# Kernel tuning notes

Measured on AMD Instinct MI355X. Metric: run time of the kernel, lower is better.

## Reference

```python
import jax, jax.numpy as jnp
import numpy as np


def _chamfer_pair(x, y):
    # x: [N,3], y: [M,3] -> per-point squared NN distances (dist1 [N], dist2 [M])
    # d_ij = |x_i|^2 + |y_j|^2 - 2 x_i . y_j
    d = (jnp.sum(x * x, axis=1)[:, None]
         + jnp.sum(y * y, axis=1)[None, :]
         - 2.0 * (x @ y.T))  # [N, M]
    return jnp.min(d, axis=1), jnp.min(d, axis=0)


def setup_inputs() -> dict:
    key = jax.random.key(0)
    k1, k2 = jax.random.split(key)
    B, N, M = 4, 8192, 8192
    xyz1 = jax.random.normal(k1, (B, N, 3), dtype=jnp.float32)
    xyz2 = jax.random.normal(k2, (B, M, 3), dtype=jnp.float32)
    return {"xyz1": xyz1, "xyz2": xyz2}


def reference(xyz1, xyz2):
    # lax.map over batch keeps peak memory to one [N,M] matrix at a time,
    # mirroring the tiled custom-kernel structure of ChamferFunction.
    dist1, dist2 = jax.lax.map(lambda ab: _chamfer_pair(ab[0], ab[1]), (xyz1, xyz2))
    return jnp.mean(dist1) + jnp.mean(dist2)
```

## Files before the change

### kernel.cpp

```cpp
#include <hip/hip_runtime.h>


#define BATCH 4
#define NPTS 8192
#define TPB 1024
#define GRID 256
#define XBLKS 32
#define YQ 2048
#define CHUNK 512
#define NCHUNK 4
#define JT 16

typedef __attribute__((ext_vector_type(8))) short bf16x8;
typedef __attribute__((ext_vector_type(16))) float f32x16;
union FragU { int4 i4; bf16x8 v; };

__device__ inline unsigned short bf16_rne(float f) {
    unsigned int u = __float_as_uint(f);
    return (unsigned short)((u + 0x7FFFu + ((u >> 16) & 1u)) >> 16);
}
__device__ inline float bf16_f32(unsigned short h) {
    return __uint_as_float(((unsigned int)h) << 16);
}
__device__ inline unsigned int pack2(unsigned int lo, unsigned int hi) {
    return (lo & 0xFFFFu) | (hi << 16);
}

__device__ inline float red16(float cb, const f32x16& d) {
    const float m0 = fminf(fminf(d[0],  d[1]),  d[2]);
    const float m1 = fminf(fminf(d[3],  d[4]),  d[5]);
    const float m2 = fminf(fminf(d[6],  d[7]),  d[8]);
    const float m3 = fminf(fminf(d[9],  d[10]), d[11]);
    const float m4 = fminf(fminf(d[12], d[13]), d[14]);
    const float u0 = fminf(fminf(m0, m1), m2);
    const float u1 = fminf(fminf(m3, m4), d[15]);
    return fminf(fminf(cb, u0), u1);
}

__device__ inline void pack_row(float x0, float x1, float x2,
                                int4& rlo, int4& rhi) {
    const unsigned short h0 = bf16_rne(x0), h1 = bf16_rne(x1), h2 = bf16_rne(x2);
    const unsigned short l0 = bf16_rne(x0 - bf16_f32(h0));
    const unsigned short l1 = bf16_rne(x1 - bf16_f32(h1));
    const unsigned short l2 = bf16_rne(x2 - bf16_f32(h2));
    const float s = x0 * x0 + x1 * x1 + x2 * x2;
    const unsigned short sh = bf16_rne(s);
    const unsigned short sl = bf16_rne(s - bf16_f32(sh));
    const unsigned short one = 0x3F80;
    rlo.x = pack2(h0, h1); rlo.y = pack2(h2, h0);
    rlo.z = pack2(h1, h2); rlo.w = pack2(l0, l1);
    rhi.x = pack2(l2, one); rhi.y = pack2(one, sh);
    rhi.z = pack2(sl, 0u);  rhi.w = 0;
}

__device__ inline void pack_col(float x0, float x1, float x2,
                                int4& clo, int4& chi) {
    const float s = x0 * x0 + x1 * x1 + x2 * x2;
    const unsigned short sh = bf16_rne(s);
    const unsigned short sl = bf16_rne(s - bf16_f32(sh));
    const float g0 = -2.0f * x0, g1 = -2.0f * x1, g2 = -2.0f * x2;
    const unsigned short gh0 = bf16_rne(g0), gh1 = bf16_rne(g1), gh2 = bf16_rne(g2);
    const unsigned short gl0 = bf16_rne(g0 - bf16_f32(gh0));
    const unsigned short gl1 = bf16_rne(g1 - bf16_f32(gh1));
    const unsigned short gl2 = bf16_rne(g2 - bf16_f32(gh2));
    const unsigned short one = 0x3F80;
    clo.x = pack2(gh0, gh1); clo.y = pack2(gh2, gl0);
    clo.z = pack2(gl1, gl2); clo.w = pack2(gh0, gh1);
    chi.x = pack2(gh2, sh);  chi.y = pack2(sl, one);
    chi.z = pack2(one, 0u);  chi.w = 0;
}

__global__ __launch_bounds__(TPB) void chamfer_one(
    const float* __restrict__ xyz1,
    const float* __restrict__ xyz2,
    unsigned long long* __restrict__ partials,
    unsigned int* __restrict__ counter,
    float* __restrict__ out)
{
    const int blk  = blockIdx.x;
    const int xblk = blk & (XBLKS - 1);
    const int b    = (blk >> 5) & (BATCH - 1);
    const int dir  = blk >> 7;

    const float* colsrc = dir ? xyz2 : xyz1;
    const float* rowsrc = dir ? xyz1 : xyz2;

    const int t    = threadIdx.x;
    const int lane = t & 63;
    const int w    = t >> 6;
    const int g    = w >> 2;
    const int wl   = w & 3;
    const int half = lane >> 5, l31 = lane & 31;

    __shared__ int4  sb0[4][CHUNK];
    __shared__ int4  sb1[4][CHUNK];
    __shared__ float part[4][256];
    __shared__ double red[16];
    __shared__ unsigned int lastflag;

    FragU bf0, bf1;
    {
        const int cbase = xblk * 256 + wl * 64 + l31;
        const float* p0 = colsrc + ((size_t)b * NPTS + cbase) * 3;
        const float* p1 = colsrc + ((size_t)b * NPTS + cbase + 32) * 3;
        int4 clo, chi;
        pack_col(p0[0], p0[1], p0[2], clo, chi);
        bf0.i4 = half ? chi : clo;
        pack_col(p1[0], p1[1], p1[2], clo, chi);
        bf1.i4 = half ? chi : clo;
    }

    float cb0 = __builtin_inff();
    float cb1 = __builtin_inff();
    const f32x16 zero = {0.0f, 0.0f, 0.0f, 0.0f, 0.0f, 0.0f, 0.0f, 0.0f,
                         0.0f, 0.0f, 0.0f, 0.0f, 0.0f, 0.0f, 0.0f, 0.0f};

    const int tid256 = t & 255;
    const int sg     = t >> 8;
    const float* rbase = rowsrc + ((size_t)b * NPTS + (size_t)sg * YQ) * 3;

    for (int c = 0; c < NCHUNK; ++c) {
        __syncthreads();
        {
            const int p = tid256 * 2;
            const float* s0 = rbase + ((size_t)c * CHUNK + p) * 3;
            int4 rlo, rhi;
            pack_row(s0[0], s0[1], s0[2], rlo, rhi);
            sb0[sg][p]     = rlo;  sb1[sg][p]     = rhi;
            pack_row(s0[3], s0[4], s0[5], rlo, rhi);
            sb0[sg][p + 1] = rlo;  sb1[sg][p + 1] = rhi;
        }
        __syncthreads();

        const int4* asrc = half ? sb1[g] : sb0[g];
#pragma unroll 4
        for (int jt = 0; jt < JT; ++jt) {
            FragU af; af.i4 = asrc[jt * 32 + l31];
            f32x16 d0 = __builtin_amdgcn_mfma_f32_32x32x16_bf16(af.v, bf0.v, zero, 0, 0, 0);
            f32x16 d1 = __builtin_amdgcn_mfma_f32_32x32x16_bf16(af.v, bf1.v, zero, 0, 0, 0);
            cb0 = red16(cb0, d0);
            cb1 = red16(cb1, d1);
        }
    }

    {
        const float v0 = fminf(cb0, __shfl_xor(cb0, 32, 64));
        const float v1 = fminf(cb1, __shfl_xor(cb1, 32, 64));
        if (half == 0) {
            part[g][wl * 64 + l31]      = v0;
            part[g][wl * 64 + 32 + l31] = v1;
        }
    }
    __syncthreads();

    double s = 0.0;
    if (t < 256) {
        const float m = fminf(fminf(part[0][t], part[1][t]),
                              fminf(part[2][t], part[3][t]));
        s = (double)m;
    }
    for (int off = 32; off > 0; off >>= 1) s += __shfl_down(s, off, 64);
    if ((t & 63) == 0) red[w] = s;
    __syncthreads();
    if (t == 0) {
        double bs = 0.0;
        for (int i = 0; i < 16; ++i) bs += red[i];
        atomicExch(&partials[blk], (unsigned long long)__double_as_longlong(bs));
        __threadfence();
        lastflag = (atomicAdd(counter, 1u) == GRID - 1) ? 1u : 0u;
    }
    __syncthreads();

    if (lastflag) {
        if (w == 0) {
            double fs = 0.0;
#pragma unroll
            for (int i = 0; i < 4; ++i) {
                const unsigned long long pv =
                    atomicAdd(&partials[lane * 4 + i], 0ull);
                fs += __longlong_as_double((long long)pv);
            }
            for (int off = 32; off > 0; off >>= 1) fs += __shfl_down(fs, off, 64);
            if (lane == 0)
                out[0] = (float)(fs / (double)(BATCH * NPTS));
        }
    }
}

extern "C" void kernel_launch(void* const* d_in, const int* in_sizes, int n_in,
                              void* d_out, int out_size, void* d_ws, size_t ws_size,
                              hipStream_t stream) {
    const float* xyz1 = (const float*)d_in[0];
    const float* xyz2 = (const float*)d_in[1];
    float* out = (float*)d_out;

    unsigned long long* partials = (unsigned long long*)d_ws;
    unsigned int* counter = (unsigned int*)(partials + GRID);

    hipMemsetAsync(counter, 0, sizeof(unsigned int), stream);

    chamfer_one<<<GRID, TPB, 0, stream>>>(xyz1, xyz2, partials, counter, out);
}
```

Baseline: 36.59 us.

## Prepack bf16 split operands in a separate kernel and stream rows from global

```diff
diff --git a/kernel.cpp b/kernel.cpp
--- a/kernel.cpp
+++ b/kernel.cpp
@@ -3,13 +3,12 @@
 
 #define BATCH 4
 #define NPTS 8192
-#define TPB 1024
-#define GRID 256
-#define XBLKS 32
-#define YQ 2048
-#define CHUNK 512
-#define NCHUNK 4
-#define JT 16
+#define TPB 512
+#define GRID 512
+#define XBLKS 64
+#define COLS_PER_BLOCK 128
+#define ROWS_PER_GROUP 2048
+#define JT 64
 
 typedef __attribute__((ext_vector_type(8))) short bf16x8;
 typedef __attribute__((ext_vector_type(16))) float f32x16;
@@ -26,6 +25,50 @@
     return (lo & 0xFFFFu) | (hi << 16);
 }
 
+__global__ __launch_bounds__(256) void prepack_kernel(
+    const float* __restrict__ xyz1, const float* __restrict__ xyz2,
+    int4* __restrict__ rowpack, int4* __restrict__ colpack,
+    unsigned int* __restrict__ counter)
+{
+    const int id  = blockIdx.x * 256 + threadIdx.x;
+    const int arr = id >> 15;
+    const int rem = id & 32767;
+    const float* p = (arr ? xyz2 : xyz1) + (size_t)rem * 3;
+    const float x0 = p[0], x1 = p[1], x2 = p[2];
+
+    if (id == 0) *counter = 0;
+
+    const unsigned short h0 = bf16_rne(x0), h1 = bf16_rne(x1), h2 = bf16_rne(x2);
+    const unsigned short l0 = bf16_rne(x0 - bf16_f32(h0));
+    const unsigned short l1 = bf16_rne(x1 - bf16_f32(h1));
+    const unsigned short l2 = bf16_rne(x2 - bf16_f32(h2));
+    const float s = x0 * x0 + x1 * x1 + x2 * x2;
+    const unsigned short sh = bf16_rne(s);
+    const unsigned short sl = bf16_rne(s - bf16_f32(sh));
+    const unsigned short one = 0x3F80;
+
+    int4 rlo, rhi;
+    rlo.x = pack2(h0, h1); rlo.y = pack2(h2, h0);
+    rlo.z = pack2(h1, h2); rlo.w = pack2(l0, l1);
+    rhi.x = pack2(l2, one); rhi.y = pack2(one, sh);
+    rhi.z = pack2(sl, 0u);  rhi.w = 0;
+    rowpack[2 * id]     = rlo;
+    rowpack[2 * id + 1] = rhi;
+
+    const float g0 = -2.0f * x0, g1 = -2.0f * x1, g2 = -2.0f * x2;
+    const unsigned short gh0 = bf16_rne(g0), gh1 = bf16_rne(g1), gh2 = bf16_rne(g2);
+    const unsigned short gl0 = bf16_rne(g0 - bf16_f32(gh0));
+    const unsigned short gl1 = bf16_rne(g1 - bf16_f32(gh1));
+    const unsigned short gl2 = bf16_rne(g2 - bf16_f32(gh2));
+    int4 clo, chi;
+    clo.x = pack2(gh0, gh1); clo.y = pack2(gh2, gl0);
+    clo.z = pack2(gl1, gl2); clo.w = pack2(gh0, gh1);
+    chi.x = pack2(gh2, sh);  chi.y = pack2(sl, one);
+    chi.z = pack2(one, 0u);  chi.w = 0;
+    colpack[2 * id]     = clo;
+    colpack[2 * id + 1] = chi;
+}
+
 __device__ inline float red16(float cb, const f32x16& d) {
     const float m0 = fminf(fminf(d[0],  d[1]),  d[2]);
     const float m1 = fminf(fminf(d[3],  d[4]),  d[5]);
@@ -37,110 +80,51 @@
     return fminf(fminf(cb, u0), u1);
 }
 
-__device__ inline void pack_row(float x0, float x1, float x2,
-                                int4& rlo, int4& rhi) {
-    const unsigned short h0 = bf16_rne(x0), h1 = bf16_rne(x1), h2 = bf16_rne(x2);
-    const unsigned short l0 = bf16_rne(x0 - bf16_f32(h0));
-    const unsigned short l1 = bf16_rne(x1 - bf16_f32(h1));
-    const unsigned short l2 = bf16_rne(x2 - bf16_f32(h2));
-    const float s = x0 * x0 + x1 * x1 + x2 * x2;
-    const unsigned short sh = bf16_rne(s);
-    const unsigned short sl = bf16_rne(s - bf16_f32(sh));
-    const unsigned short one = 0x3F80;
-    rlo.x = pack2(h0, h1); rlo.y = pack2(h2, h0);
-    rlo.z = pack2(h1, h2); rlo.w = pack2(l0, l1);
-    rhi.x = pack2(l2, one); rhi.y = pack2(one, sh);
-    rhi.z = pack2(sl, 0u);  rhi.w = 0;
-}
-
-__device__ inline void pack_col(float x0, float x1, float x2,
-                                int4& clo, int4& chi) {
-    const float s = x0 * x0 + x1 * x1 + x2 * x2;
-    const unsigned short sh = bf16_rne(s);
-    const unsigned short sl = bf16_rne(s - bf16_f32(sh));
-    const float g0 = -2.0f * x0, g1 = -2.0f * x1, g2 = -2.0f * x2;
-    const unsigned short gh0 = bf16_rne(g0), gh1 = bf16_rne(g1), gh2 = bf16_rne(g2);
-    const unsigned short gl0 = bf16_rne(g0 - bf16_f32(gh0));
-    const unsigned short gl1 = bf16_rne(g1 - bf16_f32(gh1));
-    const unsigned short gl2 = bf16_rne(g2 - bf16_f32(gh2));
-    const unsigned short one = 0x3F80;
-    clo.x = pack2(gh0, gh1); clo.y = pack2(gh2, gl0);
-    clo.z = pack2(gl1, gl2); clo.w = pack2(gh0, gh1);
-    chi.x = pack2(gh2, sh);  chi.y = pack2(sl, one);
-    chi.z = pack2(one, 0u);  chi.w = 0;
-}
-
-__global__ __launch_bounds__(TPB) void chamfer_one(
-    const float* __restrict__ xyz1,
-    const float* __restrict__ xyz2,
+__global__ __launch_bounds__(TPB) void chamfer_main(
+    const int4* __restrict__ rowpack,
+    const int4* __restrict__ colpack,
     unsigned long long* __restrict__ partials,
     unsigned int* __restrict__ counter,
     float* __restrict__ out)
 {
     const int blk  = blockIdx.x;
     const int xblk = blk & (XBLKS - 1);
-    const int b    = (blk >> 5) & (BATCH - 1);
-    const int dir  = blk >> 7;
+    const int b    = (blk >> 6) & (BATCH - 1);
+    const int dir  = blk >> 8;
+    const int arrB = dir;
+    const int arrA = dir ^ 1;
 
-    const float* colsrc = dir ? xyz2 : xyz1;
-    const float* rowsrc = dir ? xyz1 : xyz2;
-
-    const int t    = threadIdx.x;
-    const int lane = t & 63;
-    const int w    = t >> 6;
-    const int g    = w >> 2;
-    const int wl   = w & 3;
+    const int t = threadIdx.x, lane = t & 63, w = t >> 6;
+    const int g  = w >> 1;
+    const int wl = w & 1;
     const int half = lane >> 5, l31 = lane & 31;
 
-    __shared__ int4  sb0[4][CHUNK];
-    __shared__ int4  sb1[4][CHUNK];
-    __shared__ float part[4][256];
-    __shared__ double red[16];
+    __shared__ float part[4][COLS_PER_BLOCK];
+    __shared__ double red[2];
     __shared__ unsigned int lastflag;
 
+    const int cbase = xblk * COLS_PER_BLOCK + wl * 64 + l31;
+    const size_t cidx = ((size_t)(arrB * BATCH + b) * NPTS + cbase) * 2;
     FragU bf0, bf1;
-    {
-        const int cbase = xblk * 256 + wl * 64 + l31;
-        const float* p0 = colsrc + ((size_t)b * NPTS + cbase) * 3;
-        const float* p1 = colsrc + ((size_t)b * NPTS + cbase + 32) * 3;
-        int4 clo, chi;
-        pack_col(p0[0], p0[1], p0[2], clo, chi);
-        bf0.i4 = half ? chi : clo;
-        pack_col(p1[0], p1[1], p1[2], clo, chi);
-        bf1.i4 = half ? chi : clo;
-    }
+    bf0.i4 = colpack[cidx + half];
+    bf1.i4 = colpack[cidx + 64 + half];
 
     float cb0 = __builtin_inff();
     float cb1 = __builtin_inff();
     const f32x16 zero = {0.0f, 0.0f, 0.0f, 0.0f, 0.0f, 0.0f, 0.0f, 0.0f,
                          0.0f, 0.0f, 0.0f, 0.0f, 0.0f, 0.0f, 0.0f, 0.0f};
 
-    const int tid256 = t & 255;
-    const int sg     = t >> 8;
-    const float* rbase = rowsrc + ((size_t)b * NPTS + (size_t)sg * YQ) * 3;
+    const int4* asrc = rowpack
+        + ((size_t)(arrA * BATCH + b) * NPTS + (size_t)g * ROWS_PER_GROUP) * 2
+        + (size_t)l31 * 2 + half;
 
-    for (int c = 0; c < NCHUNK; ++c) {
-        __syncthreads();
-        {
-            const int p = tid256 * 2;
-            const float* s0 = rbase + ((size_t)c * CHUNK + p) * 3;
-            int4 rlo, rhi;
-            pack_row(s0[0], s0[1], s0[2], rlo, rhi);
-            sb0[sg][p]     = rlo;  sb1[sg][p]     = rhi;
-            pack_row(s0[3], s0[4], s0[5], rlo, rhi);
-            sb0[sg][p + 1] = rlo;  sb1[sg][p + 1] = rhi;
-        }
-        __syncthreads();
-
-        const int4* asrc = half ? sb1[g] : sb0[g];
 #pragma unroll 4
-        for (int jt = 0; jt < JT; ++jt) {
-            FragU af; af.i4 = asrc[jt * 32 + l31];
-            f32x16 d0 = __builtin_amdgcn_mfma_f32_32x32x16_bf16(af.v, bf0.v, zero, 0, 0, 0);
-            f32x16 d1 = __builtin_amdgcn_mfma_f32_32x32x16_bf16(af.v, bf1.v, zero, 0, 0, 0);
-            cb0 = red16(cb0, d0);
-            cb1 = red16(cb1, d1);
-        }
+    for (int jt = 0; jt < JT; ++jt) {
+        FragU af; af.i4 = asrc[(size_t)jt * 64];
+        f32x16 d0 = __builtin_amdgcn_mfma_f32_32x32x16_bf16(af.v, bf0.v, zero, 0, 0, 0);
+        f32x16 d1 = __builtin_amdgcn_mfma_f32_32x32x16_bf16(af.v, bf1.v, zero, 0, 0, 0);
+        cb0 = red16(cb0, d0);
+        cb1 = red16(cb1, d1);
     }
 
     {
@@ -154,36 +138,35 @@
     __syncthreads();
 
     double s = 0.0;
-    if (t < 256) {
+    if (t < COLS_PER_BLOCK) {
         const float m = fminf(fminf(part[0][t], part[1][t]),
                               fminf(part[2][t], part[3][t]));
         s = (double)m;
     }
-    for (int off = 32; off > 0; off >>= 1) s += __shfl_down(s, off, 64);
-    if ((t & 63) == 0) red[w] = s;
+    if (w < 2) {
+        for (int off = 32; off > 0; off >>= 1) s += __shfl_down(s, off, 64);
+        if (lane == 0) red[w] = s;
+    }
     __syncthreads();
     if (t == 0) {
-        double bs = 0.0;
-        for (int i = 0; i < 16; ++i) bs += red[i];
+        const double bs = red[0] + red[1];
         atomicExch(&partials[blk], (unsigned long long)__double_as_longlong(bs));
         __threadfence();
         lastflag = (atomicAdd(counter, 1u) == GRID - 1) ? 1u : 0u;
     }
     __syncthreads();
 
-    if (lastflag) {
-        if (w == 0) {
-            double fs = 0.0;
+    if (lastflag && w == 0) {
+        double fs = 0.0;
 #pragma unroll
-            for (int i = 0; i < 4; ++i) {
-                const unsigned long long pv =
-                    atomicAdd(&partials[lane * 4 + i], 0ull);
-                fs += __longlong_as_double((long long)pv);
-            }
-            for (int off = 32; off > 0; off >>= 1) fs += __shfl_down(fs, off, 64);
-            if (lane == 0)
-                out[0] = (float)(fs / (double)(BATCH * NPTS));
+        for (int i = 0; i < 8; ++i) {
+            const unsigned long long pv =
+                atomicAdd(&partials[lane * 8 + i], 0ull);
+            fs += __longlong_as_double((long long)pv);
         }
+        for (int off = 32; off > 0; off >>= 1) fs += __shfl_down(fs, off, 64);
+        if (lane == 0)
+            out[0] = (float)(fs / (double)(BATCH * NPTS));
     }
 }
 
@@ -194,10 +177,12 @@
     const float* xyz2 = (const float*)d_in[1];
     float* out = (float*)d_out;
 
-    unsigned long long* partials = (unsigned long long*)d_ws;
+    int4* rowpack = (int4*)d_ws;
+    int4* colpack = rowpack + 2 * 65536;
+    unsigned long long* partials = (unsigned long long*)(colpack + 2 * 65536);
     unsigned int* counter = (unsigned int*)(partials + GRID);
 
-    hipMemsetAsync(counter, 0, sizeof(unsigned int), stream);
+    prepack_kernel<<<256, 256, 0, stream>>>(xyz1, xyz2, rowpack, colpack, counter);
 
-    chamfer_one<<<GRID, TPB, 0, stream>>>(xyz1, xyz2, partials, counter, out);
+    chamfer_main<<<GRID, TPB, 0, stream>>>(rowpack, colpack, partials, counter, out);
 }
```

After: 37.21 us. No clear change (+1.7%).
